# Kernel optimization log

Hardware: AMD Instinct MI355X
Metric: run time of the kernel (lower is better)

Reference implementation:

```python
import jax, jax.numpy as jnp
import numpy as np

N_EMB = 1024
N_HEAD = 16
EPS = 1e-5


def _linear_params(key, fan_in, fan_out):
    k1, k2 = jax.random.split(key)
    lim = 1.0 / np.sqrt(fan_in)
    W = jax.random.uniform(k1, (fan_in, fan_out), minval=-lim, maxval=lim, dtype=jnp.float32)
    b = jax.random.uniform(k2, (fan_out,), minval=-lim, maxval=lim, dtype=jnp.float32)
    return W, b


def setup_inputs() -> dict:
    key = jax.random.key(0)
    ks = jax.random.split(key, 8)
    x = jax.random.normal(ks[0], (4, 2048, N_EMB), dtype=jnp.float32)
    Wk, bk = _linear_params(ks[1], N_EMB, N_EMB)
    Wq, bq = _linear_params(ks[2], N_EMB, N_EMB)
    Wv, bv = _linear_params(ks[3], N_EMB, N_EMB)
    Wp, bp = _linear_params(ks[4], N_EMB, N_EMB)
    W1, b1 = _linear_params(ks[5], N_EMB, 4 * N_EMB)
    W2, b2 = _linear_params(ks[6], 4 * N_EMB, N_EMB)
    return {
        "x": x,
        "ln1_g": jnp.ones((N_EMB,), jnp.float32), "ln1_b": jnp.zeros((N_EMB,), jnp.float32),
        "Wk": Wk, "bk": bk, "Wq": Wq, "bq": bq, "Wv": Wv, "bv": bv, "Wp": Wp, "bp": bp,
        "ln2_g": jnp.ones((N_EMB,), jnp.float32), "ln2_b": jnp.zeros((N_EMB,), jnp.float32),
        "W1": W1, "b1": b1, "W2": W2, "b2": b2,
        "cond_len": 256,
    }


def _layernorm(x, g, b):
    mu = jnp.mean(x, axis=-1, keepdims=True)
    var = jnp.mean(jnp.square(x - mu), axis=-1, keepdims=True)
    return (x - mu) * jax.lax.rsqrt(var + EPS) * g + b


def _hybrid_mask(T, cond_len):
    # rows attend to all conditioning columns; causal within the remaining block
    i = jnp.arange(T)[:, None]
    j = jnp.arange(T)[None, :]
    return (j < cond_len) | ((i >= cond_len) & (j >= cond_len) & (j <= i))  # [T,T] bool


def _block(x, ln1_g, ln1_b, Wk, bk, Wq, bq, Wv, bv, Wp, bp, ln2_g, ln2_b, W1, b1, W2, b2, cond_len):
    B, T, C = x.shape
    hd = C // N_HEAD
    h = _layernorm(x, ln1_g, ln1_b)
    # QKV: [B,T,C] -> [B,H,T,hd]
    q = (h @ Wq + bq).reshape(B, T, N_HEAD, hd).transpose(0, 2, 1, 3)
    k = (h @ Wk + bk).reshape(B, T, N_HEAD, hd).transpose(0, 2, 1, 3)
    v = (h @ Wv + bv).reshape(B, T, N_HEAD, hd).transpose(0, 2, 1, 3)
    att = jnp.einsum('bhqd,bhkd->bhqk', q, k) * (1.0 / np.sqrt(hd))
    mask = _hybrid_mask(T, cond_len)
    att = jnp.where(mask, att, -jnp.inf)
    att = jax.nn.softmax(att, axis=-1)
    y = jnp.einsum('bhqk,bhkd->bhqd', att, v)
    y = y.transpose(0, 2, 1, 3).reshape(B, T, C)
    x = x + (y @ Wp + bp)
    h2 = _layernorm(x, ln2_g, ln2_b)
    m = jax.nn.gelu(h2 @ W1 + b1, approximate=False) @ W2 + b2
    return x + m


def reference(x, ln1_g, ln1_b, Wk, bk, Wq, bq, Wv, bv, Wp, bp, ln2_g, ln2_b, W1, b1, W2, b2, cond_len):
    return _block(x, ln1_g, ln1_b, Wk, bk, Wq, bq, Wv, bv, Wp, bp, ln2_g, ln2_b, W1, b1, W2, b2, cond_len)
```

## Files before the change

kernel.cpp:

```cpp
#include <hip/hip_runtime.h>

typedef __bf16 bf16;
typedef __attribute__((ext_vector_type(4))) __bf16 bf16x4;
typedef __attribute__((ext_vector_type(8))) __bf16 bf16x8;
typedef __attribute__((ext_vector_type(4))) float f32x4;

__device__ __forceinline__ void stage16(const bf16* g, bf16* l) {
  __builtin_amdgcn_global_load_lds(
      (const __attribute__((address_space(1))) void*)g,
      (__attribute__((address_space(3))) void*)l, 16, 0, 0);
}

__global__ __launch_bounds__(256)
void transpose_f32_bf16(const float* __restrict__ src, bf16* __restrict__ dst, int R, int C)
{
  __shared__ bf16 tile[32][33];
  const int tx = threadIdx.x & 31, ty = threadIdx.x >> 5;
  const int c0 = blockIdx.x * 32, r0 = blockIdx.y * 32;
#pragma unroll
  for (int i = 0; i < 4; ++i)
    tile[ty + i * 8][tx] = (bf16)src[(size_t)(r0 + ty + i * 8) * C + c0 + tx];
  __syncthreads();
#pragma unroll
  for (int i = 0; i < 4; ++i)
    dst[(size_t)(c0 + ty + i * 8) * R + r0 + tx] = tile[tx][ty + i * 8];
}

__global__ __launch_bounds__(256)
void ln_f32_bf16(const float* __restrict__ x, const float* __restrict__ g,
                 const float* __restrict__ bta, bf16* __restrict__ out)
{
  const int row = blockIdx.x * 4 + (threadIdx.x >> 6);
  const int l = threadIdx.x & 63;
  const float* xr = x + (size_t)row * 1024 + l * 16;
  f32x4 a[4];
#pragma unroll
  for (int i = 0; i < 4; ++i) a[i] = ((const f32x4*)xr)[i];
  float s = 0.f, s2 = 0.f;
#pragma unroll
  for (int i = 0; i < 4; ++i)
#pragma unroll
    for (int jj = 0; jj < 4; ++jj) { float vv = a[i][jj]; s += vv; s2 += vv * vv; }
#pragma unroll
  for (int m = 1; m < 64; m <<= 1) { s += __shfl_xor(s, m); s2 += __shfl_xor(s2, m); }
  const float mu = s * (1.0f / 1024.0f);
  const float var = s2 * (1.0f / 1024.0f) - mu * mu;
  const float rs = rsqrtf(var + 1e-5f);
  f32x4 gv[4], bv[4];
#pragma unroll
  for (int i = 0; i < 4; ++i) {
    gv[i] = ((const f32x4*)(g + l * 16))[i];
    bv[i] = ((const f32x4*)(bta + l * 16))[i];
  }
  bf16x8 o0, o1;
#pragma unroll
  for (int i = 0; i < 8; ++i) {
    float v0 = a[i >> 2][i & 3];
    float v1 = a[2 + (i >> 2)][i & 3];
    o0[i] = (bf16)((v0 - mu) * rs * gv[i >> 2][i & 3] + bv[i >> 2][i & 3]);
    o1[i] = (bf16)((v1 - mu) * rs * gv[2 + (i >> 2)][i & 3] + bv[2 + (i >> 2)][i & 3]);
  }
  bf16* orow = out + (size_t)row * 1024 + l * 16;
  ((bf16x8*)orow)[0] = o0;
  ((bf16x8*)orow)[1] = o1;
}

template <int EPI>
__global__ __launch_bounds__(256)
void gemm_bt(const bf16* __restrict__ A, const bf16* __restrict__ Bt,
             const float* __restrict__ bias, const float* __restrict__ biasK,
             const float* __restrict__ biasV,
             void* __restrict__ out, void* __restrict__ outK, void* __restrict__ outV,
             const float* __restrict__ res, int M, int N, int K)
{
  __shared__ bf16 As[2][128 * 32];
  __shared__ bf16 Bs[2][128 * 32];
  const int tid = threadIdx.x;
  const int l = tid & 63;
  const int w = tid >> 6;
  const int wm = w >> 1, wn = w & 1;

  const unsigned nbx = gridDim.x;
  const unsigned nwg = nbx * gridDim.y;
  unsigned bid = blockIdx.x + blockIdx.y * nbx;
  const unsigned cpx = nwg >> 3;
  bid = (bid & 7) * cpx + (bid >> 3);
  const int m0 = (int)(bid % nbx) * 128;
  const int n0 = (int)(bid / nbx) * 128;

  const int srow = tid >> 2;
  const int sslot = (tid & 3) * 8;
  const bf16* gA = A + (size_t)(m0 + srow) * K + sslot;
  const bf16* gB = Bt + (size_t)(n0 + srow) * K + sslot;
  const int ldsOff = srow * 32 + sslot;

  const int lrow = l & 15;
  const int lsl8 = (l >> 4) * 8;

  f32x4 acc[4][4] = {};
  const int KT = K >> 5;

#define STAGE(buf, k0)                                        \
  do {                                                        \
    stage16(gA + (k0), &As[buf][ldsOff]);                     \
    stage16(gA + (size_t)64 * K + (k0), &As[buf][2048 + ldsOff]); \
    stage16(gB + (k0), &Bs[buf][ldsOff]);                     \
    stage16(gB + (size_t)64 * K + (k0), &Bs[buf][2048 + ldsOff]); \
  } while (0)

  STAGE(0, 0);
  __syncthreads();

  for (int kt = 0; kt < KT; ++kt) {
    const int cur = kt & 1;
    if (kt + 1 < KT) STAGE(cur ^ 1, (kt + 1) << 5);
    bf16x8 af[4], bfv[4];
#pragma unroll
    for (int i = 0; i < 4; ++i)
      af[i] = *(const bf16x8*)&As[cur][(wm * 64 + i * 16 + lrow) * 32 + lsl8];
#pragma unroll
    for (int i = 0; i < 4; ++i)
      bfv[i] = *(const bf16x8*)&Bs[cur][(wn * 64 + i * 16 + lrow) * 32 + lsl8];
#pragma unroll
    for (int mi = 0; mi < 4; ++mi)
#pragma unroll
      for (int ni = 0; ni < 4; ++ni)
        acc[mi][ni] = __builtin_amdgcn_mfma_f32_16x16x32_bf16(af[mi], bfv[ni], acc[mi][ni], 0, 0, 0);
    __syncthreads();
  }
#undef STAGE

  const int seg = n0 >> 10;
  const float* bp = (EPI == 0) ? (seg == 0 ? bias : (seg == 1 ? biasK : biasV)) : bias;
#pragma unroll
  for (int mi = 0; mi < 4; ++mi) {
#pragma unroll
    for (int ni = 0; ni < 4; ++ni) {
      const int colg = n0 + wn * 64 + ni * 16 + lrow;
      const int col = (EPI == 0) ? (colg & 1023) : colg;
      const float bv = bp[col];
#pragma unroll
      for (int j = 0; j < 4; ++j) {
        const int row = m0 + wm * 64 + mi * 16 + (l >> 4) * 4 + j;
        float val = acc[mi][ni][j] + bv;
        if constexpr (EPI == 0) {
          const int b = row >> 11, t = row & 2047, hh = col >> 6, d = col & 63;
          if (seg == 0)
            ((bf16*)out)[(((size_t)(b * 16 + hh) * 2048 + t) * 64) + d] = (bf16)(val * 0.125f);
          else if (seg == 1)
            ((bf16*)outK)[(((size_t)(b * 16 + hh) * 2048 + t) * 64) + d] = (bf16)val;
          else
            ((bf16*)outV)[(((size_t)(b * 16 + hh) * 64 + d) * 2048) + t] = (bf16)val;
        } else if constexpr (EPI == 3) {
          ((float*)out)[(size_t)row * 1024 + col] = val + res[(size_t)row * 1024 + col];
        } else if constexpr (EPI == 4) {
          const float ge = 0.5f * val * (1.0f + erff(val * 0.70710678118f));
          ((bf16*)out)[(size_t)row * N + col] = (bf16)ge;
        } else if constexpr (EPI == 5) {
          ((float*)out)[(size_t)row * 1024 + col] = val + res[(size_t)row * 1024 + col];
        }
      }
    }
  }
}

__global__ __launch_bounds__(512)
void attn_kernel(const bf16* __restrict__ q, const bf16* __restrict__ k,
                 const bf16* __restrict__ v, bf16* __restrict__ y,
                 const int* __restrict__ condp)
{
  __shared__ bf16 Ks[2][64 * 72];
  __shared__ bf16 Vs[2][64 * 72];
  __shared__ char PsB[8][2048];
  const int tid = threadIdx.x, l = tid & 63, w = tid >> 6;
  const int bx = blockIdx.x;
  const int qt = 15 - (bx >> 6);
  const int bh = bx & 63;
  const int bb = bh >> 4, hh = bh & 15;
  const int cond = condp[0];
  const int iLo = qt * 128;
  const size_t base = (size_t)bh * 2048 * 64;

  const int lrow = l & 15;
  const int g = l >> 4;
  const int lslot = g * 8;

  const int qrow = iLo + w * 16 + lrow;
  const bf16x8 bq0 = *(const bf16x8*)(q + base + (size_t)qrow * 64 + lslot);
  const bf16x8 bq1 = *(const bf16x8*)(q + base + (size_t)qrow * 64 + 32 + lslot);

  f32x4 o[4] = {};
  float m = -1e30f, lsum = 0.f;

  const int ckt = (cond + 63) >> 6;
  int nkt = ((iLo + 127) >> 6) + 1;
  if (nkt < ckt) nkt = ckt;
  const int wHi = iLo + w * 16 + 15;

  const int kr = tid >> 3;
  const int ks8 = (tid & 7) * 8;
  const bf16* kp = k + base + (size_t)kr * 64 + ks8;
  const bf16* vp = v + base + (size_t)kr * 2048 + ks8;

  bf16x8 rk = *(const bf16x8*)kp;
  bf16x8 rv = *(const bf16x8*)vp;
  *(bf16x8*)&Ks[0][kr * 72 + ks8] = rk;
  *(bf16x8*)&Vs[0][kr * 72 + ks8] = rv;
  __syncthreads();

  char* psw = PsB[w];

  for (int kt = 0; kt < nkt; ++kt) {
    const int cur = kt & 1;
    const int j0 = kt << 6;
    const bool pf = (kt + 1 < nkt);
    if (pf) {
      rk = *(const bf16x8*)(kp + (size_t)(j0 + 64) * 64);
      rv = *(const bf16x8*)(vp + j0 + 64);
    }

    const bool active = (j0 < cond) || (j0 <= wHi);
    if (active) {
      f32x4 sfr[4];
      __builtin_amdgcn_s_setprio(1);
#pragma unroll
      for (int nf = 0; nf < 4; ++nf) {
        f32x4 s = {};
        bf16x8 ka0 = *(const bf16x8*)&Ks[cur][(nf * 16 + lrow) * 72 + lslot];
        bf16x8 ka1 = *(const bf16x8*)&Ks[cur][(nf * 16 + lrow) * 72 + 32 + lslot];
        s = __builtin_amdgcn_mfma_f32_16x16x32_bf16(ka0, bq0, s, 0, 0, 0);
        s = __builtin_amdgcn_mfma_f32_16x16x32_bf16(ka1, bq1, s, 0, 0, 0);
        sfr[nf] = s;
      }
      __builtin_amdgcn_s_setprio(0);

      const bool safe = (j0 + 63 < cond) || (j0 + 63 <= iLo + w * 16);
      if (!safe) {
#pragma unroll
        for (int nf = 0; nf < 4; ++nf)
#pragma unroll
          for (int j = 0; j < 4; ++j) {
            const int kc = j0 + nf * 16 + g * 4 + j;
            const bool ok = (kc < cond) || (kc <= qrow);
            sfr[nf][j] = ok ? sfr[nf][j] : -1e30f;
          }
      }

      float pmax = sfr[0][0];
#pragma unroll
      for (int nf = 0; nf < 4; ++nf)
#pragma unroll
        for (int j = 0; j < 4; ++j) pmax = fmaxf(pmax, sfr[nf][j]);
      pmax = fmaxf(pmax, __shfl_xor(pmax, 16));
      pmax = fmaxf(pmax, __shfl_xor(pmax, 32));

      const bool resc = !__all(pmax - m <= 8.0f);
      if (resc) {
        const float mnew = fmaxf(m, pmax);
        const float alpha = __expf(m - mnew);
        m = mnew;
        lsum *= alpha;
        float ar[4];
#pragma unroll
        for (int j = 0; j < 4; ++j) ar[j] = __shfl(alpha, (l & 48) | (g * 4 + j));
#pragma unroll
        for (int df = 0; df < 4; ++df)
#pragma unroll
          for (int j = 0; j < 4; ++j) o[df][j] *= ar[j];
      }

      float rsum = 0.f;
#pragma unroll
      for (int nf = 0; nf < 4; ++nf) {
        bf16x4 pk;
#pragma unroll
        for (int j = 0; j < 4; ++j) {
          const float p = __expf(sfr[nf][j] - m);
          rsum += p;
          pk[j] = (bf16)p;
        }
        const int slot = 2 * nf + (g >> 1);
        const int boff = lrow * 128 + ((slot ^ (lrow & 7)) << 4) + (g & 1) * 8;
        *(bf16x4*)(psw + boff) = pk;
      }
      rsum += __shfl_xor(rsum, 16);
      rsum += __shfl_xor(rsum, 32);
      lsum += rsum;

      const int r0b = lrow * 128 + (((g) ^ (lrow & 7)) << 4);
      const int r1b = lrow * 128 + (((g + 4) ^ (lrow & 7)) << 4);
      const bf16x8 pa0 = *(const bf16x8*)(psw + r0b);
      const bf16x8 pa1 = *(const bf16x8*)(psw + r1b);
      __builtin_amdgcn_s_setprio(1);
#pragma unroll
      for (int df = 0; df < 4; ++df) {
        bf16x8 v0 = *(const bf16x8*)&Vs[cur][(df * 16 + lrow) * 72 + lslot];
        bf16x8 v1 = *(const bf16x8*)&Vs[cur][(df * 16 + lrow) * 72 + 32 + lslot];
        o[df] = __builtin_amdgcn_mfma_f32_16x16x32_bf16(pa0, v0, o[df], 0, 0, 0);
        o[df] = __builtin_amdgcn_mfma_f32_16x16x32_bf16(pa1, v1, o[df], 0, 0, 0);
      }
      __builtin_amdgcn_s_setprio(0);
    }

    if (pf) {
      *(bf16x8*)&Ks[cur ^ 1][kr * 72 + ks8] = rk;
      *(bf16x8*)&Vs[cur ^ 1][kr * 72 + ks8] = rv;
    }
    __syncthreads();
  }

  float lr[4];
#pragma unroll
  for (int j = 0; j < 4; ++j) lr[j] = 1.0f / __shfl(lsum, (l & 48) | (g * 4 + j));
#pragma unroll
  for (int df = 0; df < 4; ++df)
#pragma unroll
    for (int j = 0; j < 4; ++j) {
      const int irow = iLo + w * 16 + g * 4 + j;
      y[((size_t)bb * 2048 + irow) * 1024 + hh * 64 + df * 16 + lrow] = (bf16)(o[df][j] * lr[j]);
    }
}

extern "C" void kernel_launch(void* const* d_in, const int* in_sizes, int n_in,
                              void* d_out, int out_size, void* d_ws, size_t ws_size,
                              hipStream_t stream) {
  const float* x    = (const float*)d_in[0];
  const float* ln1g = (const float*)d_in[1];
  const float* ln1b = (const float*)d_in[2];
  const float* Wk   = (const float*)d_in[3];
  const float* bk   = (const float*)d_in[4];
  const float* Wq   = (const float*)d_in[5];
  const float* bq   = (const float*)d_in[6];
  const float* Wv   = (const float*)d_in[7];
  const float* bv   = (const float*)d_in[8];
  const float* Wp   = (const float*)d_in[9];
  const float* bpb  = (const float*)d_in[10];
  const float* ln2g = (const float*)d_in[11];
  const float* ln2b = (const float*)d_in[12];
  const float* W1   = (const float*)d_in[13];
  const float* b1   = (const float*)d_in[14];
  const float* W2   = (const float*)d_in[15];
  const float* b2   = (const float*)d_in[16];
  const int*  cond  = (const int*)d_in[17];
  float* out = (float*)d_out;

  char* ws = (char*)d_ws;
  const size_t MB = 1024ull * 1024ull;
  if (ws_size < 136 * MB) return;

  bf16*  WqkvT = (bf16*)(ws + 0 * MB);
  bf16*  WpT   = (bf16*)(ws + 6 * MB);
  bf16*  W1T   = (bf16*)(ws + 8 * MB);
  bf16*  W2T   = (bf16*)(ws + 16 * MB);
  float* x2    = (float*)(ws + 24 * MB);
  bf16*  hbuf  = (bf16*)(ws + 56 * MB);
  bf16*  qb    = (bf16*)(ws + 72 * MB);
  bf16*  kb    = (bf16*)(ws + 88 * MB);
  bf16*  vb    = (bf16*)(ws + 104 * MB);
  bf16*  yb    = (bf16*)(ws + 120 * MB);
  bf16*  m1    = (bf16*)(ws + 72 * MB);

  dim3 blk(256);
  transpose_f32_bf16<<<dim3(32, 32), blk, 0, stream>>>(Wq, WqkvT,                1024, 1024);
  transpose_f32_bf16<<<dim3(32, 32), blk, 0, stream>>>(Wk, WqkvT + 1024 * 1024,  1024, 1024);
  transpose_f32_bf16<<<dim3(32, 32), blk, 0, stream>>>(Wv, WqkvT + 2048 * 1024,  1024, 1024);
  transpose_f32_bf16<<<dim3(32, 32), blk, 0, stream>>>(Wp, WpT, 1024, 1024);
  transpose_f32_bf16<<<dim3(128, 32), blk, 0, stream>>>(W1, W1T, 1024, 4096);
  transpose_f32_bf16<<<dim3(32, 128), blk, 0, stream>>>(W2, W2T, 4096, 1024);

  ln_f32_bf16<<<2048, blk, 0, stream>>>(x, ln1g, ln1b, hbuf);

  gemm_bt<0><<<dim3(64, 24), blk, 0, stream>>>(hbuf, WqkvT, bq, bk, bv,
                                               qb, kb, vb, nullptr, 8192, 3072, 1024);

  attn_kernel<<<dim3(1024), dim3(512), 0, stream>>>(qb, kb, vb, yb, cond);

  gemm_bt<3><<<dim3(64, 8), blk, 0, stream>>>(yb, WpT, bpb, nullptr, nullptr,
                                              x2, nullptr, nullptr, x, 8192, 1024, 1024);
  ln_f32_bf16<<<2048, blk, 0, stream>>>(x2, ln2g, ln2b, hbuf);
  gemm_bt<4><<<dim3(64, 32), blk, 0, stream>>>(hbuf, W1T, b1, nullptr, nullptr,
                                               m1, nullptr, nullptr, nullptr, 8192, 4096, 1024);
  gemm_bt<5><<<dim3(64, 8), blk, 0, stream>>>(m1, W2T, b2, nullptr, nullptr,
                                              out, nullptr, nullptr, x2, 8192, 1024, 4096);
}
```

Baseline: 457.0 us.

## Swizzle GEMM LDS layout, use explicit vmcnt waits, drop XCD block remap

Applies an XOR swizzle to the LDS column slot, on both the global source address and the fragment reads, to reduce LDS bank conflicts. It replaces __syncthreads with raw s_barrier plus explicit s_waitcnt vmcnt, so the prefetch of the next tile can stay in flight while the current one is consumed. It also removes the XCD-aware block index remapping and uses plain blockIdx mapping, which may reduce L2 locality across chiplets.

```diff
diff --git a/kernel.cpp b/kernel.cpp
--- a/kernel.cpp
+++ b/kernel.cpp
@@ -79,54 +79,55 @@
   const int l = tid & 63;
   const int w = tid >> 6;
   const int wm = w >> 1, wn = w & 1;
-
-  const unsigned nbx = gridDim.x;
-  const unsigned nwg = nbx * gridDim.y;
-  unsigned bid = blockIdx.x + blockIdx.y * nbx;
-  const unsigned cpx = nwg >> 3;
-  bid = (bid & 7) * cpx + (bid >> 3);
-  const int m0 = (int)(bid % nbx) * 128;
-  const int n0 = (int)(bid / nbx) * 128;
+  const int m0 = blockIdx.x * 128;
+  const int n0 = blockIdx.y * 128;
 
   const int srow = tid >> 2;
-  const int sslot = (tid & 3) * 8;
-  const bf16* gA = A + (size_t)(m0 + srow) * K + sslot;
-  const bf16* gB = Bt + (size_t)(n0 + srow) * K + sslot;
-  const int ldsOff = srow * 32 + sslot;
+  const int sG8 = ((tid & 3) ^ ((tid >> 3) & 3)) * 8;
+  const bf16* gA = A + (size_t)(m0 + srow) * K + sG8;
+  const bf16* gB = Bt + (size_t)(n0 + srow) * K + sG8;
+  const int ldsOff = srow * 32 + (tid & 3) * 8;
 
   const int lrow = l & 15;
-  const int lsl8 = (l >> 4) * 8;
+  const int rdsl = ((l >> 4) ^ ((lrow >> 1) & 3)) * 8;
 
   f32x4 acc[4][4] = {};
   const int KT = K >> 5;
 
-#define STAGE(buf, k0)                                        \
-  do {                                                        \
-    stage16(gA + (k0), &As[buf][ldsOff]);                     \
+#define STAGE(buf, k0)                                            \
+  do {                                                            \
+    stage16(gA + (k0), &As[buf][ldsOff]);                         \
     stage16(gA + (size_t)64 * K + (k0), &As[buf][2048 + ldsOff]); \
-    stage16(gB + (k0), &Bs[buf][ldsOff]);                     \
+    stage16(gB + (k0), &Bs[buf][ldsOff]);                         \
     stage16(gB + (size_t)64 * K + (k0), &Bs[buf][2048 + ldsOff]); \
   } while (0)
 
   STAGE(0, 0);
-  __syncthreads();
 
   for (int kt = 0; kt < KT; ++kt) {
     const int cur = kt & 1;
-    if (kt + 1 < KT) STAGE(cur ^ 1, (kt + 1) << 5);
+    __builtin_amdgcn_s_barrier();
+    if (kt + 1 < KT) {
+      STAGE(cur ^ 1, (kt + 1) << 5);
+      asm volatile("s_waitcnt vmcnt(4)" ::: "memory");
+    } else {
+      asm volatile("s_waitcnt vmcnt(0)" ::: "memory");
+    }
+    __builtin_amdgcn_sched_barrier(0);
+    __builtin_amdgcn_s_barrier();
+
     bf16x8 af[4], bfv[4];
 #pragma unroll
     for (int i = 0; i < 4; ++i)
-      af[i] = *(const bf16x8*)&As[cur][(wm * 64 + i * 16 + lrow) * 32 + lsl8];
+      af[i] = *(const bf16x8*)&As[cur][(wm * 64 + i * 16 + lrow) * 32 + rdsl];
 #pragma unroll
     for (int i = 0; i < 4; ++i)
-      bfv[i] = *(const bf16x8*)&Bs[cur][(wn * 64 + i * 16 + lrow) * 32 + lsl8];
+      bfv[i] = *(const bf16x8*)&Bs[cur][(wn * 64 + i * 16 + lrow) * 32 + rdsl];
 #pragma unroll
     for (int mi = 0; mi < 4; ++mi)
 #pragma unroll
       for (int ni = 0; ni < 4; ++ni)
         acc[mi][ni] = __builtin_amdgcn_mfma_f32_16x16x32_bf16(af[mi], bfv[ni], acc[mi][ni], 0, 0, 0);
-    __syncthreads();
   }
 #undef STAGE
 
```

Measured after the change: 413.8 us. -9.4%, faster.
